# Kernel tuning notes

Hardware: AMD Instinct MI355X
Metric: run time of the kernel (lower is better)

## Reference

```python
import jax, jax.numpy as jnp
import numpy as np
from math import sqrt

B, L, D, H = 2, 2048, 1024, 16
DH = D // H


def setup_inputs() -> dict:
    key = jax.random.key(0)
    ks = jax.random.split(key, 12)
    s = 1.0 / sqrt(D)
    inp = {
        'q': jax.random.normal(ks[0], (B, L, D), jnp.float32),
        'k': jax.random.normal(ks[1], (B, L, D), jnp.float32),
        'v': jax.random.normal(ks[2], (B, L, D), jnp.float32),
        'mask': jnp.zeros((B, 1, L, L), dtype=bool),
        'Wq': jax.random.normal(ks[3], (D, D), jnp.float32) * s,
        'bq': jnp.zeros((D,), jnp.float32),
        'Wk': jax.random.normal(ks[4], (D, D), jnp.float32) * s,
        'bk': jnp.zeros((D,), jnp.float32),
        'Wv': jax.random.normal(ks[5], (D, D), jnp.float32) * s,
        'bv': jnp.zeros((D,), jnp.float32),
        'Wo': jax.random.normal(ks[6], (D, D), jnp.float32) * s,
        'bo': jnp.zeros((D,), jnp.float32),
    }
    return inp


def _split(x):
    # [B, L, D] -> [B, H, L, DH]
    b, l, _ = x.shape
    return x.reshape(b, l, H, DH).transpose(0, 2, 1, 3)


def reference(q, k, v, mask, Wq, bq, Wk, bk, Wv, bv, Wo, bo):
    qh = _split(q @ Wq.T + bq)
    kh = _split(k @ Wk.T + bk)
    vh = _split(v @ Wv.T + bv)
    scores = jnp.einsum('bhqd,bhkd->bhqk', qh, kh) / sqrt(DH)
    scores = jnp.where(mask, -jnp.inf, scores)
    attn = jax.nn.softmax(scores, axis=-1)
    out = jnp.einsum('bhqk,bhkd->bhqd', attn, vh)
    out = out.transpose(0, 2, 1, 3).reshape(q.shape[0], -1, D)
    return out @ Wo.T + bo
```

## Files before the change

kernel.cpp:

```cpp
#include <hip/hip_runtime.h>
#include <hip/hip_bf16.h>
#include <stdint.h>

#define B_    2
#define L_    2048
#define D_    1024
#define H_    16
#define DH_   64
#define MTOT  (B_ * L_)

typedef __attribute__((ext_vector_type(8)))  short short8;
typedef __attribute__((ext_vector_type(4)))  float f32x4;
typedef __attribute__((ext_vector_type(16))) float f32x16;
typedef __attribute__((ext_vector_type(4)))  unsigned int u32x4;

static __device__ __forceinline__ short f2bf(float f) {
    uint32_t u = __builtin_bit_cast(uint32_t, f);
    uint32_t r = (u + 0x7fffu + ((u >> 16) & 1u)) >> 16;
    return (short)r;
}

static __device__ __forceinline__ void load_lds16(const short* g, short* l) {
    __builtin_amdgcn_global_load_lds(
        (const __attribute__((address_space(1))) unsigned int*)g,
        (__attribute__((address_space(3))) unsigned int*)l,
        16, 0, 0);
}

__global__ __launch_bounds__(256) void cvt_all(
        const float* __restrict__ s0, const float* __restrict__ s1,
        const float* __restrict__ s2, const float* __restrict__ s3,
        const float* __restrict__ s4, const float* __restrict__ s5,
        const float* __restrict__ s6,
        short* __restrict__ d0, short* __restrict__ d1, short* __restrict__ d2,
        short* __restrict__ d3, short* __restrict__ d4, short* __restrict__ d5,
        short* __restrict__ d6) {
    const int y = blockIdx.y;
    if (y >= 3 && blockIdx.x >= 512) return;
    const float* s; short* d;
    switch (y) {
        case 0: s = s0; d = d0; break;
        case 1: s = s1; d = d1; break;
        case 2: s = s2; d = d2; break;
        case 3: s = s3; d = d3; break;
        case 4: s = s4; d = d4; break;
        case 5: s = s5; d = d5; break;
        default: s = s6; d = d6; break;
    }
    size_t i = ((size_t)blockIdx.x * 256 + threadIdx.x) * 8;
    float4 x = *(const float4*)(s + i);
    float4 yv = *(const float4*)(s + i + 4);
    short8 o;
    o[0] = f2bf(x.x); o[1] = f2bf(x.y); o[2] = f2bf(x.z); o[3] = f2bf(x.w);
    o[4] = f2bf(yv.x); o[5] = f2bf(yv.y); o[6] = f2bf(yv.z); o[7] = f2bf(yv.w);
    *(short8*)(d + i) = o;
}

template <typename OutT>
static __device__ __forceinline__ void gemm_bt_body(
        const short* __restrict__ A, const short* __restrict__ W,
        const float* __restrict__ bias, OutT* __restrict__ C, float oscale) {
    constexpr int K = 1024, N = 1024;
    __shared__ short As[2][128 * 32];
    __shared__ short Ws[2][128 * 32];
    const int tid  = threadIdx.x;
    const int wid  = tid >> 6;
    const int lane = tid & 63;
    const int wr = wid >> 1, wc = wid & 1;
    const int g = lane >> 4, r = lane & 15;

    const int hid = blockIdx.y * 8 + blockIdx.x;
    const int bid = (hid & 7) * 32 + (hid >> 3);
    const int rowbase = (bid >> 3) * 128;
    const int colbase = (bid & 7) * 128;

    const int c0   = wid * 64 + lane;
    const int srow = c0 >> 2;
    const int scol = (c0 & 3) * 8;
    const short* Abase = A + (size_t)(rowbase + srow) * K + scol;
    const short* Wbase = W + (size_t)(colbase + srow) * K + scol;

    auto stage = [&](int buf, int k0) {
#pragma unroll
        for (int i = 0; i < 2; i++) {
            load_lds16(Abase + (size_t)i * 64 * K + k0,
                       &As[buf][(i * 256 + wid * 64) * 8]);
            load_lds16(Wbase + (size_t)i * 64 * K + k0,
                       &Ws[buf][(i * 256 + wid * 64) * 8]);
        }
    };

    f32x4 acc[4][4] = {};

    stage(0, 0);
    __syncthreads();

    for (int k0 = 0; k0 < K; k0 += 32) {
        const int cur = (k0 >> 5) & 1, nxt = cur ^ 1;
        if (k0 + 32 < K) stage(nxt, k0 + 32);

        short8 af[4], bf[4];
#pragma unroll
        for (int mi = 0; mi < 4; mi++)
            af[mi] = *(const short8*)&As[cur][(wr * 64 + mi * 16 + r) * 32 + g * 8];
#pragma unroll
        for (int ni = 0; ni < 4; ni++)
            bf[ni] = *(const short8*)&Ws[cur][(wc * 64 + ni * 16 + r) * 32 + g * 8];
#pragma unroll
        for (int mi = 0; mi < 4; mi++)
#pragma unroll
            for (int ni = 0; ni < 4; ni++)
                acc[mi][ni] = __builtin_amdgcn_mfma_f32_16x16x32_bf16(
                    af[mi], bf[ni], acc[mi][ni], 0, 0, 0);
        __syncthreads();
    }

#pragma unroll
    for (int mi = 0; mi < 4; mi++)
#pragma unroll
        for (int ni = 0; ni < 4; ni++) {
            int row0 = rowbase + wr * 64 + mi * 16 + g * 4;
            int col  = colbase + wc * 64 + ni * 16 + r;
            float bb = bias[col];
#pragma unroll
            for (int t = 0; t < 4; t++) {
                float val = (acc[mi][ni][t] + bb) * oscale;
                size_t idx = (size_t)(row0 + t) * N + col;
                if constexpr (__is_same(OutT, short)) C[idx] = f2bf(val);
                else                                  C[idx] = val;
            }
        }
}

__global__ __launch_bounds__(256) void gemm_proj3(
        const short* __restrict__ Qa, const short* __restrict__ Ka, const short* __restrict__ Va,
        const short* __restrict__ Wq, const short* __restrict__ Wk, const short* __restrict__ Wv,
        const float* __restrict__ bq, const float* __restrict__ bk, const float* __restrict__ bv,
        short* __restrict__ Qo, short* __restrict__ Ko, short* __restrict__ Vo, float qscale) {
    const short* A; const short* W; const float* bias; short* C; float sc;
    if (blockIdx.z == 0)      { A = Qa; W = Wq; bias = bq; C = Qo; sc = qscale; }
    else if (blockIdx.z == 1) { A = Ka; W = Wk; bias = bk; C = Ko; sc = 1.0f; }
    else                      { A = Va; W = Wv; bias = bv; C = Vo; sc = 1.0f; }
    gemm_bt_body<short>(A, W, bias, C, sc);
}

__global__ __launch_bounds__(256) void gemm_out(
        const short* __restrict__ A, const short* __restrict__ W,
        const float* __restrict__ bias, float* __restrict__ C) {
    gemm_bt_body<float>(A, W, bias, C, 1.0f);
}

__global__ __launch_bounds__(512, 4) void attn_kernel(
        const short* __restrict__ Qp, const short* __restrict__ Kp,
        const short* __restrict__ Vp, short* __restrict__ Ao) {
    const int hwx = blockIdx.x, hwy = blockIdx.y;
    const int bh    = (hwx & 7) * 4 + (hwy & 3);
    const int qtile = (hwy >> 2) * 2 + (hwx >> 3);
    const int b  = bh >> 4;
    const int h  = bh & 15;
    const int q0 = qtile * 128;
    const int tid = threadIdx.x;
    const int w   = tid >> 6;
    const int l   = tid & 63;
    const int l31 = l & 31;
    const int hi  = l >> 5;
    const int kg  = w >> 2;
    const int qw  = w & 3;
    const size_t rowbase = (size_t)b * L_;
    const int kbase = kg * (L_ / 2);

    __shared__ short KS[2][2][64 * 64];
    __shared__ short VT[2][2][64 * 64];

    const int qrow = q0 + qw * 32 + l31;
    short8 qf[4];
    {
        const short* qptr = Qp + (rowbase + qrow) * D_ + h * 64 + hi * 8;
#pragma unroll
        for (int s16 = 0; s16 < 4; s16++)
            qf[s16] = *(const short8*)(qptr + s16 * 16);
    }

    f32x16 o0 = {0.f,0.f,0.f,0.f,0.f,0.f,0.f,0.f,0.f,0.f,0.f,0.f,0.f,0.f,0.f,0.f};
    f32x16 o1 = o0;
    float lpart = 0.f;

    const int rsw = l31 & 7;
    int qkoff[4];
#pragma unroll
    for (int s16 = 0; s16 < 4; s16++)
        qkoff[s16] = ((s16 * 2 + hi) ^ rsw) << 4;
    const int rowb0 = l31 * 128;
    const int rowb1 = (32 + l31) * 128;
    const int vsw = ((l31 & 7) << 4) ^ (((l31 >> 3) & 3) << 5);
    int voff[2][2];
#pragma unroll
    for (int ks = 0; ks < 2; ks++)
#pragma unroll
        for (int kk = 0; kk < 2; kk++)
            voff[ks][kk] = (ks * 64 + kk * 32 + hi * 16) ^ vsw;

    const short* kbase_p = Kp + (rowbase + kbase + qw * 8 + (l >> 3)) * D_ +
                           h * 64 + (((l & 7) ^ ((l >> 3) & 7)) * 8);
    auto stageK = [&](int buf, int t) {
        const short* src = kbase_p + (size_t)t * 64 * D_;
        short* dst = &KS[kg][buf][qw * 512];
        load_lds16(src, dst);
        load_lds16(src + (size_t)32 * D_, dst + 2048);
    };

    const int gt = tid & 255;
    const int pr = gt >> 3;
    const int c0 = gt & 7;
    const int spr = (pr & 0x19) | ((pr & 2) << 1) | ((pr & 4) >> 1);
    const int svbase = (spr * 4) ^ ((c0 & 3) << 5);
    const short* vptr = Vp + (rowbase + kbase + 2 * pr) * D_ + h * 64 + c0 * 8;

    short8 vr0, vr1;
    auto loadV = [&](int t) {
        const size_t off = (size_t)t * 64 * D_;
        vr0 = *(const short8*)(vptr + off);
        vr1 = *(const short8*)(vptr + off + D_);
    };
    auto writeVt = [&](int buf) {
        char* Vt = (char*)&VT[kg][buf][0];
        u32x4 w0 = __builtin_bit_cast(u32x4, vr0);
        u32x4 w1 = __builtin_bit_cast(u32x4, vr1);
#pragma unroll
        for (int jj = 0; jj < 8; jj++) {
            uint32_t pk = __builtin_amdgcn_perm(
                w0[jj >> 1], w1[jj >> 1],
                (jj & 1) ? 0x03020706u : 0x01000504u);
            *(uint32_t*)(Vt + c0 * 1024 + jj * 128 + (svbase ^ (jj << 4))) = pk;
        }
    };

    auto qk = [&](const char* ksb, int ks) -> f32x16 {
        f32x16 s = {0.f,0.f,0.f,0.f,0.f,0.f,0.f,0.f,0.f,0.f,0.f,0.f,0.f,0.f,0.f,0.f};
        const char* kb = ksb + ks * 4096 + rowb0;
        __builtin_amdgcn_s_setprio(1);
#pragma unroll
        for (int s16 = 0; s16 < 4; s16++) {
            short8 kf = *(const short8*)(kb + qkoff[s16]);
            s = __builtin_amdgcn_mfma_f32_32x32x16_bf16(kf, qf[s16], s, 0, 0, 0);
        }
        __builtin_amdgcn_s_setprio(0);
        return s;
    };

    auto smpv = [&](f32x16 s, int ks, const char* vtb) {
#pragma unroll
        for (int i = 0; i < 16; i++) s[i] = __builtin_amdgcn_exp2f(s[i]);
        {
            float t0 = (s[0] + s[1]) + (s[2] + s[3]);
            float t1 = (s[4] + s[5]) + (s[6] + s[7]);
            float t2 = (s[8] + s[9]) + (s[10] + s[11]);
            float t3 = (s[12] + s[13]) + (s[14] + s[15]);
            lpart += (t0 + t1) + (t2 + t3);
        }
        uint32_t wd[8];
#pragma unroll
        for (int i = 0; i < 8; i++)
            asm("v_cvt_pk_bf16_f32 %0, %1, %2"
                : "=v"(wd[i]) : "v"(s[2 * i]), "v"(s[2 * i + 1]));
        u32x4 a0 = { wd[0], wd[1], wd[2], wd[3] };
        u32x4 a1 = { wd[4], wd[5], wd[6], wd[7] };
        short8 pf0 = __builtin_bit_cast(short8, a0);
        short8 pf1 = __builtin_bit_cast(short8, a1);
        __builtin_amdgcn_s_setprio(1);
#pragma unroll
        for (int kk = 0; kk < 2; kk++) {
            short8 pf = (kk == 0) ? pf0 : pf1;
            short8 vf0 = *(const short8*)(vtb + rowb0 + voff[ks][kk]);
            o0 = __builtin_amdgcn_mfma_f32_32x32x16_bf16(pf, vf0, o0, 0, 0, 0);
            short8 vf1 = *(const short8*)(vtb + rowb1 + voff[ks][kk]);
            o1 = __builtin_amdgcn_mfma_f32_32x32x16_bf16(pf, vf1, o1, 0, 0, 0);
        }
        __builtin_amdgcn_s_setprio(0);
    };

    stageK(0, 0);
    loadV(0);
    writeVt(0);
    __syncthreads();

    constexpr int NT = (L_ / 2) / 64;
    for (int t = 0; t < NT; t++) {
        const int cur = t & 1, nxt = cur ^ 1;
        const bool pre = (t + 1 < NT);
        if (pre) {
            stageK(nxt, t + 1);
            loadV(t + 1);
        }
        const char* ksb = (const char*)&KS[kg][cur][0];
        const char* vtb = (const char*)&VT[kg][cur][0];
        f32x16 sA = qk(ksb, 0);
        f32x16 sB = qk(ksb, 1);
        smpv(sA, 0, vtb);
        smpv(sB, 1, vtb);
        if (pre) writeVt(nxt);
        __syncthreads();
    }

    float lrow = lpart + __shfl_xor(lpart, 32, 64);

    float* mrgO = (float*)&KS[0][0][0];
    float* mrgL = (float*)&VT[0][0][0];
    const int idx = qw * 64 + l;
    if (kg == 1) {
#pragma unroll
        for (int i = 0; i < 16; i++) {
            mrgO[i * 256 + idx]        = o0[i];
            mrgO[(16 + i) * 256 + idx] = o1[i];
        }
        mrgL[idx] = lrow;
    }
    __syncthreads();
    if (kg == 0) {
        float lsum = lrow + mrgL[idx];
#pragma unroll
        for (int rr = 0; rr < 16; rr++) {
            int crow  = (rr & 3) + 8 * (rr >> 2) + 4 * hi;
            float lq  = __shfl(lsum, crow, 64);
            float inv = 1.0f / lq;
            float v0 = (o0[rr] + mrgO[rr * 256 + idx])        * inv;
            float v1 = (o1[rr] + mrgO[(16 + rr) * 256 + idx]) * inv;
            int row = q0 + qw * 32 + crow;
            size_t base = (rowbase + row) * D_ + h * 64 + l31;
            Ao[base]      = f2bf(v0);
            Ao[base + 32] = f2bf(v1);
        }
    }
}

extern "C" void kernel_launch(void* const* d_in, const int* in_sizes, int n_in,
                              void* d_out, int out_size, void* d_ws, size_t ws_size,
                              hipStream_t stream) {
    const float* q  = (const float*)d_in[0];
    const float* k  = (const float*)d_in[1];
    const float* v  = (const float*)d_in[2];
    const float* Wq = (const float*)d_in[4];
    const float* bq = (const float*)d_in[5];
    const float* Wk = (const float*)d_in[6];
    const float* bk = (const float*)d_in[7];
    const float* Wv = (const float*)d_in[8];
    const float* bv = (const float*)d_in[9];
    const float* Wo = (const float*)d_in[10];
    const float* bo = (const float*)d_in[11];
    float* out = (float*)d_out;

    char* ws = (char*)d_ws;
    const size_t SZ_ACT = (size_t)MTOT * D_ * sizeof(short);
    const size_t SZ_W   = (size_t)D_ * D_ * sizeof(short);
    short* Qb  = (short*)(ws);
    short* Kb  = (short*)(ws + SZ_ACT);
    short* Vb  = (short*)(ws + 2 * SZ_ACT);
    short* Wqb = (short*)(ws + 3 * SZ_ACT);
    short* Wkb = (short*)(ws + 3 * SZ_ACT + SZ_W);
    short* Wvb = (short*)(ws + 3 * SZ_ACT + 2 * SZ_W);
    short* Wob = (short*)(ws + 3 * SZ_ACT + 3 * SZ_W);
    short* Qp  = (short*)(ws + 3 * SZ_ACT + 4 * SZ_W);
    short* Kp  = (short*)(ws + 4 * SZ_ACT + 4 * SZ_W);
    short* Vp  = (short*)(ws + 5 * SZ_ACT + 4 * SZ_W);
    short* Ao  = Qb;

    const float qscale = 0.125f * 1.4426950408889634f;

    cvt_all<<<dim3(2048, 7, 1), 256, 0, stream>>>(
        q, k, v, Wq, Wk, Wv, Wo, Qb, Kb, Vb, Wqb, Wkb, Wvb, Wob);
    gemm_proj3<<<dim3(8, 32, 3), 256, 0, stream>>>(Qb, Kb, Vb, Wqb, Wkb, Wvb,
                                                   bq, bk, bv, Qp, Kp, Vp, qscale);
    attn_kernel<<<dim3(16, 32, 1), 512, 0, stream>>>(Qp, Kp, Vp, Ao);
    gemm_out<<<dim3(8, 32, 1), 256, 0, stream>>>(Ao, Wob, bo, out);
}
```

Baseline: 125.0 us.

## Fuse fp32-to-bf16 activation conversion into projection GEMM and re-lay out V LDS

The projection GEMM now loads the fp32 q/k/v activations directly into registers, converts them to bf16 and writes them to LDS. The separate conversion kernel therefore only handles the weights, which removes a full write-and-reread of three bf16 activation buffers. The attention kernel also replaces the XOR-swizzled transposed V tile with a padded row stride, with rotated write order and split 8-byte reads, and changes the K swizzle to reduce LDS bank conflicts. The cost is higher register pressure and synchronous global loads in the GEMM A path instead of asynchronous direct-to-LDS loads.

```diff
diff --git a/kernel.cpp b/kernel.cpp
--- a/kernel.cpp
+++ b/kernel.cpp
@@ -12,6 +12,7 @@
 typedef __attribute__((ext_vector_type(8)))  short short8;
 typedef __attribute__((ext_vector_type(4)))  float f32x4;
 typedef __attribute__((ext_vector_type(16))) float f32x16;
+typedef __attribute__((ext_vector_type(2)))  unsigned int u32x2;
 typedef __attribute__((ext_vector_type(4)))  unsigned int u32x4;
 
 static __device__ __forceinline__ short f2bf(float f) {
@@ -27,25 +28,17 @@
         16, 0, 0);
 }
 
-__global__ __launch_bounds__(256) void cvt_all(
+__global__ __launch_bounds__(256) void cvt_w(
         const float* __restrict__ s0, const float* __restrict__ s1,
         const float* __restrict__ s2, const float* __restrict__ s3,
-        const float* __restrict__ s4, const float* __restrict__ s5,
-        const float* __restrict__ s6,
-        short* __restrict__ d0, short* __restrict__ d1, short* __restrict__ d2,
-        short* __restrict__ d3, short* __restrict__ d4, short* __restrict__ d5,
-        short* __restrict__ d6) {
-    const int y = blockIdx.y;
-    if (y >= 3 && blockIdx.x >= 512) return;
+        short* __restrict__ d0, short* __restrict__ d1,
+        short* __restrict__ d2, short* __restrict__ d3) {
     const float* s; short* d;
-    switch (y) {
+    switch (blockIdx.y) {
         case 0: s = s0; d = d0; break;
         case 1: s = s1; d = d1; break;
         case 2: s = s2; d = d2; break;
-        case 3: s = s3; d = d3; break;
-        case 4: s = s4; d = d4; break;
-        case 5: s = s5; d = d5; break;
-        default: s = s6; d = d6; break;
+        default: s = s3; d = d3; break;
     }
     size_t i = ((size_t)blockIdx.x * 256 + threadIdx.x) * 8;
     float4 x = *(const float4*)(s + i);
@@ -56,9 +49,9 @@
     *(short8*)(d + i) = o;
 }
 
-template <typename OutT>
+template <typename OutT, bool AF32>
 static __device__ __forceinline__ void gemm_bt_body(
-        const short* __restrict__ A, const short* __restrict__ W,
+        const void* __restrict__ Av, const short* __restrict__ W,
         const float* __restrict__ bias, OutT* __restrict__ C, float oscale) {
     constexpr int K = 1024, N = 1024;
     __shared__ short As[2][128 * 32];
@@ -77,27 +70,63 @@
     const int c0   = wid * 64 + lane;
     const int srow = c0 >> 2;
     const int scol = (c0 & 3) * 8;
-    const short* Abase = A + (size_t)(rowbase + srow) * K + scol;
+    const short* Abase  = AF32 ? nullptr
+                               : (const short*)Av + (size_t)(rowbase + srow) * K + scol;
+    const float* A32base = AF32 ? (const float*)Av + (size_t)(rowbase + srow) * K + scol
+                                : nullptr;
     const short* Wbase = W + (size_t)(colbase + srow) * K + scol;
 
+    float4 afl[4];
+
     auto stage = [&](int buf, int k0) {
 #pragma unroll
         for (int i = 0; i < 2; i++) {
-            load_lds16(Abase + (size_t)i * 64 * K + k0,
-                       &As[buf][(i * 256 + wid * 64) * 8]);
+            if constexpr (!AF32)
+                load_lds16(Abase + (size_t)i * 64 * K + k0,
+                           &As[buf][(i * 256 + wid * 64) * 8]);
             load_lds16(Wbase + (size_t)i * 64 * K + k0,
                        &Ws[buf][(i * 256 + wid * 64) * 8]);
         }
     };
+    auto stageA_load = [&](int k0) {
+        if constexpr (AF32) {
+#pragma unroll
+            for (int i = 0; i < 2; i++) {
+                afl[i * 2 + 0] = *(const float4*)(A32base + (size_t)i * 64 * K + k0);
+                afl[i * 2 + 1] = *(const float4*)(A32base + (size_t)i * 64 * K + k0 + 4);
+            }
+        }
+    };
+    auto stageA_write = [&](int buf) {
+        if constexpr (AF32) {
+#pragma unroll
+            for (int i = 0; i < 2; i++) {
+                uint32_t w0, w1, w2, w3;
+                asm("v_cvt_pk_bf16_f32 %0, %1, %2"
+                    : "=v"(w0) : "v"(afl[i * 2].x), "v"(afl[i * 2].y));
+                asm("v_cvt_pk_bf16_f32 %0, %1, %2"
+                    : "=v"(w1) : "v"(afl[i * 2].z), "v"(afl[i * 2].w));
+                asm("v_cvt_pk_bf16_f32 %0, %1, %2"
+                    : "=v"(w2) : "v"(afl[i * 2 + 1].x), "v"(afl[i * 2 + 1].y));
+                asm("v_cvt_pk_bf16_f32 %0, %1, %2"
+                    : "=v"(w3) : "v"(afl[i * 2 + 1].z), "v"(afl[i * 2 + 1].w));
+                u32x4 v = { w0, w1, w2, w3 };
+                *(u32x4*)&As[buf][(i * 256 + wid * 64 + lane) * 8] = v;
+            }
+        }
+    };
 
     f32x4 acc[4][4] = {};
 
+    stageA_load(0);
     stage(0, 0);
+    stageA_write(0);
     __syncthreads();
 
     for (int k0 = 0; k0 < K; k0 += 32) {
         const int cur = (k0 >> 5) & 1, nxt = cur ^ 1;
-        if (k0 + 32 < K) stage(nxt, k0 + 32);
+        const bool pre = (k0 + 32 < K);
+        if (pre) { stage(nxt, k0 + 32); stageA_load(k0 + 32); }
 
         short8 af[4], bf[4];
 #pragma unroll
@@ -112,6 +141,7 @@
             for (int ni = 0; ni < 4; ni++)
                 acc[mi][ni] = __builtin_amdgcn_mfma_f32_16x16x32_bf16(
                     af[mi], bf[ni], acc[mi][ni], 0, 0, 0);
+        if (pre) stageA_write(nxt);
         __syncthreads();
     }
 
@@ -133,22 +163,24 @@
 }
 
 __global__ __launch_bounds__(256) void gemm_proj3(
-        const short* __restrict__ Qa, const short* __restrict__ Ka, const short* __restrict__ Va,
+        const float* __restrict__ Qa, const float* __restrict__ Ka, const float* __restrict__ Va,
         const short* __restrict__ Wq, const short* __restrict__ Wk, const short* __restrict__ Wv,
         const float* __restrict__ bq, const float* __restrict__ bk, const float* __restrict__ bv,
         short* __restrict__ Qo, short* __restrict__ Ko, short* __restrict__ Vo, float qscale) {
-    const short* A; const short* W; const float* bias; short* C; float sc;
+    const float* A; const short* W; const float* bias; short* C; float sc;
     if (blockIdx.z == 0)      { A = Qa; W = Wq; bias = bq; C = Qo; sc = qscale; }
     else if (blockIdx.z == 1) { A = Ka; W = Wk; bias = bk; C = Ko; sc = 1.0f; }
     else                      { A = Va; W = Wv; bias = bv; C = Vo; sc = 1.0f; }
-    gemm_bt_body<short>(A, W, bias, C, sc);
+    gemm_bt_body<short, true>(A, W, bias, C, sc);
 }
 
 __global__ __launch_bounds__(256) void gemm_out(
         const short* __restrict__ A, const short* __restrict__ W,
         const float* __restrict__ bias, float* __restrict__ C) {
-    gemm_bt_body<float>(A, W, bias, C, 1.0f);
-}
+    gemm_bt_body<float, false>(A, W, bias, C, 1.0f);
+}
+
+#define VSTRIDE 136
 
 __global__ __launch_bounds__(512, 4) void attn_kernel(
         const short* __restrict__ Qp, const short* __restrict__ Kp,
@@ -170,7 +202,7 @@
     const int kbase = kg * (L_ / 2);
 
     __shared__ short KS[2][2][64 * 64];
-    __shared__ short VT[2][2][64 * 64];
+    __shared__ short VT[2][2][64 * (VSTRIDE/2)];
 
     const int qrow = q0 + qw * 32 + l31;
     short8 qf[4];
@@ -185,23 +217,24 @@
     f32x16 o1 = o0;
     float lpart = 0.f;
 
-    const int rsw = l31 & 7;
+    const int sigma = (l31 & 7) ^ (((l31 >> 3) & 3) << 1);
     int qkoff[4];
 #pragma unroll
     for (int s16 = 0; s16 < 4; s16++)
-        qkoff[s16] = ((s16 * 2 + hi) ^ rsw) << 4;
-    const int rowb0 = l31 * 128;
-    const int rowb1 = (32 + l31) * 128;
-    const int vsw = ((l31 & 7) << 4) ^ (((l31 >> 3) & 3) << 5);
+        qkoff[s16] = ((s16 * 2 + hi) ^ sigma) << 4;
+    const int krowb  = l31 * 128;
+    const int vrowb0 = l31 * VSTRIDE;
+    const int vrowb1 = (32 + l31) * VSTRIDE;
     int voff[2][2];
 #pragma unroll
     for (int ks = 0; ks < 2; ks++)
 #pragma unroll
         for (int kk = 0; kk < 2; kk++)
-            voff[ks][kk] = (ks * 64 + kk * 32 + hi * 16) ^ vsw;
-
+            voff[ks][kk] = ks * 64 + kk * 32 + hi * 16;
+
+    const int kslot = (l & 7) ^ (l >> 3) ^ ((qw & 3) << 1);
     const short* kbase_p = Kp + (rowbase + kbase + qw * 8 + (l >> 3)) * D_ +
-                           h * 64 + (((l & 7) ^ ((l >> 3) & 7)) * 8);
+                           h * 64 + kslot * 8;
     auto stageK = [&](int buf, int t) {
         const short* src = kbase_p + (size_t)t * 64 * D_;
         short* dst = &KS[kg][buf][qw * 512];
@@ -213,7 +246,6 @@
     const int pr = gt >> 3;
     const int c0 = gt & 7;
     const int spr = (pr & 0x19) | ((pr & 2) << 1) | ((pr & 4) >> 1);
-    const int svbase = (spr * 4) ^ ((c0 & 3) << 5);
     const short* vptr = Vp + (rowbase + kbase + 2 * pr) * D_ + h * 64 + c0 * 8;
 
     short8 vr0, vr1;
@@ -228,16 +260,24 @@
         u32x4 w1 = __builtin_bit_cast(u32x4, vr1);
 #pragma unroll
         for (int jj = 0; jj < 8; jj++) {
+            const int je = (jj + c0) & 7;
             uint32_t pk = __builtin_amdgcn_perm(
-                w0[jj >> 1], w1[jj >> 1],
-                (jj & 1) ? 0x03020706u : 0x01000504u);
-            *(uint32_t*)(Vt + c0 * 1024 + jj * 128 + (svbase ^ (jj << 4))) = pk;
-        }
+                w0[je >> 1], w1[je >> 1],
+                (je & 1) ? 0x03020706u : 0x01000504u);
+            *(uint32_t*)(Vt + (c0 * 8 + je) * VSTRIDE + spr * 4) = pk;
+        }
+    };
+
+    auto vload = [&](const char* vtb, int rowb, int off) -> short8 {
+        u32x2 a = *(const u32x2*)(vtb + rowb + off);
+        u32x2 bq_ = *(const u32x2*)(vtb + rowb + off + 8);
+        u32x4 c = { a[0], a[1], bq_[0], bq_[1] };
+        return __builtin_bit_cast(short8, c);
     };
 
     auto qk = [&](const char* ksb, int ks) -> f32x16 {
         f32x16 s = {0.f,0.f,0.f,0.f,0.f,0.f,0.f,0.f,0.f,0.f,0.f,0.f,0.f,0.f,0.f,0.f};
-        const char* kb = ksb + ks * 4096 + rowb0;
+        const char* kb = ksb + ks * 4096 + krowb;
         __builtin_amdgcn_s_setprio(1);
 #pragma unroll
         for (int s16 = 0; s16 < 4; s16++) {
@@ -271,9 +311,9 @@
 #pragma unroll
         for (int kk = 0; kk < 2; kk++) {
             short8 pf = (kk == 0) ? pf0 : pf1;
-            short8 vf0 = *(const short8*)(vtb + rowb0 + voff[ks][kk]);
+            short8 vf0 = vload(vtb, vrowb0, voff[ks][kk]);
             o0 = __builtin_amdgcn_mfma_f32_32x32x16_bf16(pf, vf0, o0, 0, 0, 0);
-            short8 vf1 = *(const short8*)(vtb + rowb1 + voff[ks][kk]);
+            short8 vf1 = vload(vtb, vrowb1, voff[ks][kk]);
             o1 = __builtin_amdgcn_mfma_f32_32x32x16_bf16(pf, vf1, o1, 0, 0, 0);
         }
         __builtin_amdgcn_s_setprio(0);
@@ -352,9 +392,7 @@
     char* ws = (char*)d_ws;
     const size_t SZ_ACT = (size_t)MTOT * D_ * sizeof(short);
     const size_t SZ_W   = (size_t)D_ * D_ * sizeof(short);
-    short* Qb  = (short*)(ws);
-    short* Kb  = (short*)(ws + SZ_ACT);
-    short* Vb  = (short*)(ws + 2 * SZ_ACT);
+    short* Ao  = (short*)(ws);
     short* Wqb = (short*)(ws + 3 * SZ_ACT);
     short* Wkb = (short*)(ws + 3 * SZ_ACT + SZ_W);
     short* Wvb = (short*)(ws + 3 * SZ_ACT + 2 * SZ_W);
@@ -362,13 +400,12 @@
     short* Qp  = (short*)(ws + 3 * SZ_ACT + 4 * SZ_W);
     short* Kp  = (short*)(ws + 4 * SZ_ACT + 4 * SZ_W);
     short* Vp  = (short*)(ws + 5 * SZ_ACT + 4 * SZ_W);
-    short* Ao  = Qb;
 
     const float qscale = 0.125f * 1.4426950408889634f;
 
-    cvt_all<<<dim3(2048, 7, 1), 256, 0, stream>>>(
-        q, k, v, Wq, Wk, Wv, Wo, Qb, Kb, Vb, Wqb, Wkb, Wvb, Wob);
-    gemm_proj3<<<dim3(8, 32, 3), 256, 0, stream>>>(Qb, Kb, Vb, Wqb, Wkb, Wvb,
+    cvt_w<<<dim3(512, 4, 1), 256, 0, stream>>>(Wq, Wk, Wv, Wo,
+                                               Wqb, Wkb, Wvb, Wob);
+    gemm_proj3<<<dim3(8, 32, 3), 256, 0, stream>>>(q, k, v, Wqb, Wkb, Wvb,
                                                    bq, bk, bv, Qp, Kp, Vp, qscale);
     attn_kernel<<<dim3(16, 32, 1), 512, 0, stream>>>(Qp, Kp, Vp, Ao);
     gemm_out<<<dim3(8, 32, 1), 256, 0, stream>>>(Ao, Wob, bo, out);
```

Result: slower. 131.7 us (+5.4%).
